# Kernel tuning notes

Hardware: AMD Instinct MI355X
Metric: run time of the kernel (lower is better)

## Reference

```python
import jax, jax.numpy as jnp
import numpy as np


def setup_inputs() -> dict:
    key = jax.random.key(0)
    k1, k2, k3 = jax.random.split(key, 3)
    B, D, F = 4096, 1024, 16384  # batch, input_dim, dict_size
    x = jax.random.normal(k1, (B, D), dtype=jnp.float32)
    W_enc = jax.random.normal(k2, (F, D), dtype=jnp.float32) * (1.0 / np.sqrt(D))
    b_enc = jnp.zeros((F,), dtype=jnp.float32)
    W_dec = jax.random.normal(k3, (D, F), dtype=jnp.float32)
    # decoder columns are unit-normalized (as in _normalize_decoder)
    W_dec = W_dec / jnp.clip(jnp.linalg.norm(W_dec, axis=0, keepdims=True), 1e-8)
    b_dec = jnp.zeros((D,), dtype=jnp.float32)
    return {"x": x, "W_enc": W_enc, "b_enc": b_enc, "W_dec": W_dec, "b_dec": b_dec, "k": 32}


def reference(x, W_enc, b_enc, W_dec, b_dec, k):
    # encode: z_pre = (x - b_dec) @ W_enc^T + b_enc   -> [B, F]
    x_centered = x - b_dec
    z_pre = jnp.einsum('bd,fd->bf', x_centered, W_enc) + b_enc
    # activate: TopK(ReLU(z_pre)) via top_k + relu + scatter
    topk_vals, topk_idx = jax.lax.top_k(z_pre, k)           # [B, k]
    B = z_pre.shape[0]
    rows = jnp.arange(B)[:, None]                            # [B, 1]
    z = jnp.zeros_like(z_pre).at[rows, topk_idx].set(jax.nn.relu(topk_vals))
    # decode: x_hat = z @ W_dec^T + b_dec (dense matmul over sparse z)
    x_hat = jnp.einsum('bf,df->bd', z, W_dec) + b_dec
    return (x_hat, z, z_pre)
```

## Files before the change

### kernel.cpp

```cpp
#include <hip/hip_runtime.h>
#include <cstdint>
#include <cfloat>
#include <cstddef>

#define MAXK 128

typedef __attribute__((ext_vector_type(8))) short bf16x8;
typedef __attribute__((ext_vector_type(4))) float f32x4;

__device__ __forceinline__ void split8(const float4& v0, const float4& v1,
                                       uint4& hp, uint4& lp)
{
    float vv[8] = {v0.x, v0.y, v0.z, v0.w, v1.x, v1.y, v1.z, v1.w};
    unsigned h[8], l[8];
    #pragma unroll
    for (int i = 0; i < 8; ++i) {
        unsigned u  = __float_as_uint(vv[i]);
        unsigned hb = u & 0xFFFF0000u;
        float lf    = vv[i] - __uint_as_float(hb);
        h[i] = u;
        l[i] = __float_as_uint(lf);
    }
    hp.x = (h[0] >> 16) | (h[1] & 0xFFFF0000u);
    hp.y = (h[2] >> 16) | (h[3] & 0xFFFF0000u);
    hp.z = (h[4] >> 16) | (h[5] & 0xFFFF0000u);
    hp.w = (h[6] >> 16) | (h[7] & 0xFFFF0000u);
    lp.x = (l[0] >> 16) | (l[1] & 0xFFFF0000u);
    lp.y = (l[2] >> 16) | (l[3] & 0xFFFF0000u);
    lp.z = (l[4] >> 16) | (l[5] & 0xFFFF0000u);
    lp.w = (l[6] >> 16) | (l[7] & 0xFFFF0000u);
}

__device__ __forceinline__ void gload_lds16(const void* g, void* l)
{
    __builtin_amdgcn_global_load_lds(
        (const __attribute__((address_space(1))) unsigned int*)g,
        (__attribute__((address_space(3))) unsigned int*)l,
        16, 0, 0);
}

__global__ __launch_bounds__(256)
void prep_x_kernel(const float* __restrict__ x, const float* __restrict__ b_dec,
                   ushort* __restrict__ AhiP, ushort* __restrict__ AloP, int D)
{
    const int c   = blockIdx.x * 256 + threadIdx.x;
    const int t   = c >> 9;
    const int wc  = c & 511;
    const int rl  = wc >> 2;
    const int pkc = wc & 3;
    const int kc  = (pkc - (rl >> 1)) & 3;
    const int nkb = D >> 5;
    const int band = t / nkb, kblk = t - band * nkb;
    const int row = band * 128 + rl;
    const int k0  = kblk * 32 + kc * 8;

    const float* src = x + (size_t)row * D + k0;
    float4 v0 = *(const float4*)(src);
    float4 v1 = *(const float4*)(src + 4);
    const float* bd = b_dec + k0;
    float4 d0 = *(const float4*)(bd);
    float4 d1 = *(const float4*)(bd + 4);
    v0.x -= d0.x; v0.y -= d0.y; v0.z -= d0.z; v0.w -= d0.w;
    v1.x -= d1.x; v1.y -= d1.y; v1.z -= d1.z; v1.w -= d1.w;
    uint4 hp, lp;
    split8(v0, v1, hp, lp);
    const size_t off = (size_t)t * 4096 + (size_t)wc * 8;
    *(uint4*)&AhiP[off] = hp;
    *(uint4*)&AloP[off] = lp;
}

__global__ __launch_bounds__(256)
void prep_w_kernel(const float* __restrict__ Wenc,
                   ushort* __restrict__ WhiP, ushort* __restrict__ WloP, int D)
{
    const int c   = blockIdx.x * 256 + threadIdx.x;
    const int t   = c >> 10;
    const int wc  = c & 1023;
    const int rl  = wc >> 2;
    const int pkc = wc & 3;
    const int kc  = (pkc - (rl >> 1)) & 3;
    const int nkb = D >> 5;
    const int fband = t / nkb, kblk = t - fband * nkb;
    const int f   = fband * 256 + rl;
    const int k0  = kblk * 32 + kc * 8;

    const float* src = Wenc + (size_t)f * D + k0;
    float4 v0 = *(const float4*)(src);
    float4 v1 = *(const float4*)(src + 4);
    uint4 hp, lp;
    split8(v0, v1, hp, lp);
    const size_t off = (size_t)t * 8192 + (size_t)wc * 8;
    *(uint4*)&WhiP[off] = hp;
    *(uint4*)&WloP[off] = lp;
}

__global__ __launch_bounds__(256, 2)
void encode_gemm_pre(const ushort* __restrict__ AhiP, const ushort* __restrict__ AloP,
                     const ushort* __restrict__ WhiP, const ushort* __restrict__ WloP,
                     const float* __restrict__ b_enc, float* __restrict__ z_pre,
                     int D, int F)
{
    __shared__ ushort AsHi[4096];
    __shared__ ushort AsLo[4096];
    __shared__ ushort BsHi[8192];
    __shared__ ushort BsLo[8192];

    const int tid = threadIdx.x;
    const int bm  = blockIdx.y * 128;
    const int bn  = blockIdx.x * 256;

    const int lane = tid & 63;
    const int w    = tid >> 6;
    const int wm   = (w >> 1) * 64;
    const int wn   = (w & 1) * 128;
    const int fr   = lane & 15;
    const int q    = lane >> 4;
    const int nkb  = D >> 5;

    int aoff[4], boff[8];
    #pragma unroll
    for (int mi = 0; mi < 4; ++mi) {
        const int r = wm + mi * 16 + fr;
        aoff[mi] = r * 32 + (((q + (r >> 1)) & 3) * 8);
    }
    #pragma unroll
    for (int ni = 0; ni < 8; ++ni) {
        const int r = wn + ni * 16 + fr;
        boff[ni] = r * 32 + (((q + (r >> 1)) & 3) * 8);
    }

    f32x4 acc[4][8];
    #pragma unroll
    for (int mi = 0; mi < 4; ++mi)
        #pragma unroll
        for (int ni = 0; ni < 8; ++ni)
            acc[mi][ni] = (f32x4){0.f, 0.f, 0.f, 0.f};

    const char* aHi = (const char*)AhiP + (size_t)blockIdx.y * nkb * 8192;
    const char* aLo = (const char*)AloP + (size_t)blockIdx.y * nkb * 8192;
    const char* bHi = (const char*)WhiP + (size_t)blockIdx.x * nkb * 16384;
    const char* bLo = (const char*)WloP + (size_t)blockIdx.x * nkb * 16384;
    const int la16 = lane * 16;

    for (int kb = 0; kb < nkb; ++kb) {
        const char* pa = aHi + (size_t)kb * 8192;
        const char* pl = aLo + (size_t)kb * 8192;
        const char* pb = bHi + (size_t)kb * 16384;
        const char* pm = bLo + (size_t)kb * 16384;

        #pragma unroll
        for (int c = 0; c < 2; ++c) {
            const int off = (w * 2 + c) * 1024;
            gload_lds16(pa + off + la16, (char*)AsHi + off);
            gload_lds16(pl + off + la16, (char*)AsLo + off);
        }
        #pragma unroll
        for (int c = 0; c < 4; ++c) {
            const int off = (w * 4 + c) * 1024;
            gload_lds16(pb + off + la16, (char*)BsHi + off);
            gload_lds16(pm + off + la16, (char*)BsLo + off);
        }
        asm volatile("s_waitcnt vmcnt(0)" ::: "memory");
        __syncthreads();

        bf16x8 ahi[4], alo[4];
        #pragma unroll
        for (int mi = 0; mi < 4; ++mi) {
            ahi[mi] = *(const bf16x8*)&AsHi[aoff[mi]];
            alo[mi] = *(const bf16x8*)&AsLo[aoff[mi]];
        }
        #pragma unroll
        for (int ni = 0; ni < 8; ++ni) {
            bf16x8 bhi = *(const bf16x8*)&BsHi[boff[ni]];
            bf16x8 blo = *(const bf16x8*)&BsLo[boff[ni]];
            #pragma unroll
            for (int mi = 0; mi < 4; ++mi) {
                acc[mi][ni] = __builtin_amdgcn_mfma_f32_16x16x32_bf16(alo[mi], bhi, acc[mi][ni], 0, 0, 0);
                acc[mi][ni] = __builtin_amdgcn_mfma_f32_16x16x32_bf16(ahi[mi], blo, acc[mi][ni], 0, 0, 0);
                acc[mi][ni] = __builtin_amdgcn_mfma_f32_16x16x32_bf16(ahi[mi], bhi, acc[mi][ni], 0, 0, 0);
            }
        }
        __syncthreads();
    }

    #pragma unroll
    for (int ni = 0; ni < 8; ++ni) {
        const int col = bn + wn + ni * 16 + fr;
        const float be = b_enc[col];
        #pragma unroll
        for (int mi = 0; mi < 4; ++mi) {
            const int rbase = bm + wm + mi * 16 + q * 4;
            float* dst = z_pre + (size_t)rbase * F + col;
            #pragma unroll
            for (int r = 0; r < 4; ++r)
                dst[(size_t)r * F] = acc[mi][ni][r] + be;
        }
    }
}

__global__ __launch_bounds__(256, 2)
void encode_gemm_bf16x3(const float* __restrict__ x, const float* __restrict__ Wenc,
                        const float* __restrict__ b_enc, const float* __restrict__ b_dec,
                        float* __restrict__ z_pre, int D, int F)
{
    constexpr int BM = 128, BN = 256, BK = 32;
    __shared__ ushort AsHi[BM * BK];
    __shared__ ushort AsLo[BM * BK];
    __shared__ ushort BsHi[BN * BK];
    __shared__ ushort BsLo[BN * BK];

    const int tid = threadIdx.x;
    const int bm  = blockIdx.y * BM;
    const int bn  = blockIdx.x * BN;

    const int lane = tid & 63;
    const int w    = tid >> 6;
    const int wm   = (w >> 1) * 64;
    const int wn   = (w & 1) * 128;
    const int fr   = lane & 15;
    const int q    = lane >> 4;

    int aoff[4], boff[8];
    #pragma unroll
    for (int mi = 0; mi < 4; ++mi) {
        const int r = wm + mi * 16 + fr;
        aoff[mi] = r * 32 + (((q + (r >> 1)) & 3) * 8);
    }
    #pragma unroll
    for (int ni = 0; ni < 8; ++ni) {
        const int r = wn + ni * 16 + fr;
        boff[ni] = r * 32 + (((q + (r >> 1)) & 3) * 8);
    }

    f32x4 acc[4][8];
    #pragma unroll
    for (int mi = 0; mi < 4; ++mi)
        #pragma unroll
        for (int ni = 0; ni < 8; ++ni)
            acc[mi][ni] = (f32x4){0.f, 0.f, 0.f, 0.f};

    for (int k0 = 0; k0 < D; k0 += BK) {
        #pragma unroll
        for (int j = 0; j < 2; ++j) {
            const int task = tid + 256 * j;
            const int row = task >> 2, kc = task & 3;
            const float* src = x + (size_t)(bm + row) * D + k0 + kc * 8;
            float4 v0 = *(const float4*)(src);
            float4 v1 = *(const float4*)(src + 4);
            const float* bd = b_dec + k0 + kc * 8;
            float4 d0 = *(const float4*)(bd);
            float4 d1 = *(const float4*)(bd + 4);
            v0.x -= d0.x; v0.y -= d0.y; v0.z -= d0.z; v0.w -= d0.w;
            v1.x -= d1.x; v1.y -= d1.y; v1.z -= d1.z; v1.w -= d1.w;
            uint4 hp, lp;
            split8(v0, v1, hp, lp);
            const int off = row * 32 + (((kc + (row >> 1)) & 3) * 8);
            *(uint4*)&AsHi[off] = hp;
            *(uint4*)&AsLo[off] = lp;
        }
        #pragma unroll
        for (int j = 0; j < 4; ++j) {
            const int task = tid + 256 * j;
            const int row = task >> 2, kc = task & 3;
            const float* src = Wenc + (size_t)(bn + row) * D + k0 + kc * 8;
            float4 v0 = *(const float4*)(src);
            float4 v1 = *(const float4*)(src + 4);
            uint4 hp, lp;
            split8(v0, v1, hp, lp);
            const int off = row * 32 + (((kc + (row >> 1)) & 3) * 8);
            *(uint4*)&BsHi[off] = hp;
            *(uint4*)&BsLo[off] = lp;
        }
        __syncthreads();

        bf16x8 ahi[4], alo[4];
        #pragma unroll
        for (int mi = 0; mi < 4; ++mi) {
            ahi[mi] = *(const bf16x8*)&AsHi[aoff[mi]];
            alo[mi] = *(const bf16x8*)&AsLo[aoff[mi]];
        }
        #pragma unroll
        for (int ni = 0; ni < 8; ++ni) {
            bf16x8 bhi = *(const bf16x8*)&BsHi[boff[ni]];
            bf16x8 blo = *(const bf16x8*)&BsLo[boff[ni]];
            #pragma unroll
            for (int mi = 0; mi < 4; ++mi) {
                acc[mi][ni] = __builtin_amdgcn_mfma_f32_16x16x32_bf16(alo[mi], bhi, acc[mi][ni], 0, 0, 0);
                acc[mi][ni] = __builtin_amdgcn_mfma_f32_16x16x32_bf16(ahi[mi], blo, acc[mi][ni], 0, 0, 0);
                acc[mi][ni] = __builtin_amdgcn_mfma_f32_16x16x32_bf16(ahi[mi], bhi, acc[mi][ni], 0, 0, 0);
            }
        }
        __syncthreads();
    }

    #pragma unroll
    for (int ni = 0; ni < 8; ++ni) {
        const int col = bn + wn + ni * 16 + fr;
        const float be = b_enc[col];
        #pragma unroll
        for (int mi = 0; mi < 4; ++mi) {
            const int rbase = bm + wm + mi * 16 + q * 4;
            float* dst = z_pre + (size_t)rbase * F + col;
            #pragma unroll
            for (int r = 0; r < 4; ++r)
                dst[(size_t)r * F] = acc[mi][ni][r] + be;
        }
    }
}

__device__ __forceinline__ unsigned fkey(float f)
{
    unsigned u = __float_as_uint(f);
    return u ^ ((unsigned)((int)u >> 31) | 0x80000000u);
}
__device__ __forceinline__ float finv(unsigned k)
{
    unsigned u = (k & 0x80000000u) ? (k ^ 0x80000000u) : ~k;
    return __uint_as_float(u);
}

__device__ __forceinline__ float exact_zpre(const float* __restrict__ xr,
                                            const float* __restrict__ Wenc,
                                            const float* __restrict__ b_enc,
                                            const float* __restrict__ b_dec,
                                            int f, int D, int ln)
{
    const float* wr = Wenc + (size_t)f * D;
    float s = 0.f;
    for (int d = ln * 4; d < D; d += 256) {
        float4 xv = *(const float4*)(xr + d);
        float4 bd = *(const float4*)(b_dec + d);
        float4 wv4 = *(const float4*)(wr + d);
        s = fmaf(xv.x - bd.x, wv4.x, s);
        s = fmaf(xv.y - bd.y, wv4.y, s);
        s = fmaf(xv.z - bd.z, wv4.z, s);
        s = fmaf(xv.w - bd.w, wv4.w, s);
    }
    #pragma unroll
    for (int o = 32; o > 0; o >>= 1) s += __shfl_down(s, o, 64);
    return s + b_enc[f];
}

#define DLT 4e-3f

template <int NVEC>
__global__ __launch_bounds__(256)
void topk_fast(const float* __restrict__ z_pre, float* __restrict__ z,
               float* __restrict__ ws_vals, int* __restrict__ ws_idx,
               const int* __restrict__ k_ptr,
               const float* __restrict__ x, const float* __restrict__ Wenc,
               const float* __restrict__ b_enc, const float* __restrict__ b_dec,
               int F, int D)
{
    const int row = blockIdx.x;
    const int t   = threadIdx.x;
    const int k   = *k_ptr;
    const int nv4 = F >> 2;
    const int wv_id = t >> 6, ln = t & 63;

    __shared__ ushort keys[16384];
    __shared__ float  cand_v[256];
    __shared__ int    cand_i[256];
    __shared__ unsigned char cand_sel[256];
    __shared__ int    bnd[128];
    __shared__ float  s2w[4];
    __shared__ int    hist4[4][256];
    __shared__ int    waveTot[4];
    __shared__ int    s_bin, s_above;
    __shared__ int    n_c_s, n_b_s, c_hi_s, out_cnt, cnt_tau_s, bad_s;
    __shared__ unsigned vk_key;

    if (t == 0) {
        n_c_s = 0; n_b_s = 0; c_hi_s = 0; out_cnt = 0; cnt_tau_s = 0; bad_s = 0;
        vk_key = 0xFFFFFFFFu;
    }

    const float*  zrow = z_pre + (size_t)row * F;
    const float4* src  = (const float4*)zrow;
    float4* dstz = (float4*)(z + (size_t)row * F);
    const float4 zz = make_float4(0.f, 0.f, 0.f, 0.f);

    float s2 = 0.f;
    #pragma unroll
    for (int i = 0; i < NVEC; ++i) {
        const int p = t + 256 * i;
        if (p < nv4) {
            const float4 v = src[p];
            dstz[p] = zz;
            const unsigned k0 = fkey(v.x) >> 16;
            const unsigned k1 = fkey(v.y) >> 16;
            const unsigned k2 = fkey(v.z) >> 16;
            const unsigned k3 = fkey(v.w) >> 16;
            uint2 pk;
            pk.x = k0 | (k1 << 16);
            pk.y = k2 | (k3 << 16);
            *(uint2*)&keys[p * 4] = pk;
            s2 = fmaf(v.x, v.x, s2);
            s2 = fmaf(v.y, v.y, s2);
            s2 = fmaf(v.z, v.z, s2);
            s2 = fmaf(v.w, v.w, s2);
        }
    }
    #pragma unroll
    for (int o = 32; o > 0; o >>= 1) s2 += __shfl_down(s2, o, 64);
    if (ln == 0) s2w[wv_id] = s2;
    __syncthreads();

    const float sigma = sqrtf((s2w[0] + s2w[1] + s2w[2] + s2w[3]) / (float)F);
    int c0 = 4 * k; if (c0 < 64) c0 = 64; if (c0 > 192) c0 = 192;
    const float qq  = (float)c0 / (float)F;
    const float tt  = sqrtf(-2.f * logf(qq));
    const float phi = tt - (2.30753f + 0.27061f * tt) /
                           (1.f + 0.99229f * tt + 0.04481f * tt * tt);
    const float tau = sigma * phi;
    const unsigned tk = fkey(tau) >> 16;
    const unsigned tkey16 = (tk >= 2) ? (tk - 2) : 0;

    const int nU = nv4 * 2;
    const unsigned* keysU = (const unsigned*)keys;
    for (int j = t; j < nU; j += 256) {
        const unsigned pr = keysU[j];
        const unsigned ka = pr & 0xFFFFu, kb = pr >> 16;
        if (ka > tkey16) { const int s = atomicAdd(&n_c_s, 1); if (s < 256) cand_i[s] = 2 * j; }
        if (kb > tkey16) { const int s = atomicAdd(&n_c_s, 1); if (s < 256) cand_i[s] = 2 * j + 1; }
    }
    __syncthreads();

    if (t == 0 && (n_c_s > 256 || !(tau > 0.1f))) bad_s = 1;
    const int n_c = min(n_c_s, 256);

    float myv = 0.f;
    if (t < n_c) {
        myv = zrow[cand_i[t]];
        cand_v[t] = myv;
        if (myv > tau) atomicAdd(&cnt_tau_s, 1);
    }
    __syncthreads();
    if (t == 0 && cnt_tau_s < k) bad_s = 1;

    cand_sel[t] = 0;
    if (t < n_c) {
        int gt = 0;
        for (int j = 0; j < n_c; ++j) gt += (cand_v[j] > myv);
        if (gt <= k - 1) atomicMin(&vk_key, fkey(myv));
    }
    __syncthreads();

    const float vkv = finv(vk_key);
    if (t < n_c) {
        if (myv > vkv + DLT) {
            cand_sel[t] = 2;
            atomicAdd(&c_hi_s, 1);
        } else if (myv > vkv - DLT) {
            const int sb = atomicAdd(&n_b_s, 1);
            if (sb < 128) bnd[sb] = t;
        }
    }
    __syncthreads();
    if (t == 0 && n_b_s > 128) bad_s = 1;
    __syncthreads();

    if (!bad_s) {
        const int n_b = n_b_s;
        const float* xr = x + (size_t)row * D;
        for (int b2 = wv_id; b2 < n_b; b2 += 4) {
            const int c = bnd[b2];
            const float ex = exact_zpre(xr, Wenc, b_enc, b_dec, cand_i[c], D, ln);
            if (ln == 0) cand_v[c] = ex;
        }
        __syncthreads();

        if (t == 0) {
            int need = k - c_hi_s;
            if (need > n_b) need = n_b;
            for (int it = 0; it < need; ++it) {
                int bi = -1; float bv = 0.f;
                for (int b2 = 0; b2 < n_b; ++b2) {
                    const int c = bnd[b2];
                    if (cand_sel[c]) continue;
                    const float v = cand_v[c];
                    if (bi < 0 || v > bv || (v == bv && cand_i[c] < cand_i[bi])) {
                        bi = c; bv = v;
                    }
                }
                if (bi < 0) break;
                cand_sel[bi] = 1;
            }
        }
        __syncthreads();

        float* wvp = ws_vals + (size_t)row * MAXK;
        int*   wip = ws_idx  + (size_t)row * MAXK;
        if (t < n_c && cand_sel[t]) {
            const float zv = fmaxf(cand_v[t], 0.f);
            z[(size_t)row * F + cand_i[t]] = zv;
            const int s = atomicAdd(&out_cnt, 1);
            if (s < MAXK) { wvp[s] = zv; wip[s] = cand_i[t]; }
        }
        return;
    }

    if (t == 0) { n_c_s = 0; c_hi_s = 0; out_cnt = 0; }
    __syncthreads();

    unsigned prefix = 0;
    int rem = k;
    for (int pass = 0; pass < 2; ++pass) {
        const int shift = 24 - 8 * pass;
        hist4[0][t] = 0; hist4[1][t] = 0; hist4[2][t] = 0; hist4[3][t] = 0;
        __syncthreads();
        for (int j = t; j < F; j += 256) {
            const unsigned key = fkey(zrow[j]);
            const bool inb = (pass == 0) || ((key >> (shift + 8)) == prefix);
            if (inb) atomicAdd(&hist4[wv_id][(key >> shift) & 255], 1);
        }
        __syncthreads();
        const int cnt = hist4[0][t] + hist4[1][t] + hist4[2][t] + hist4[3][t];
        int s = cnt;
        #pragma unroll
        for (int off = 1; off < 64; off <<= 1) {
            const int tmp = __shfl_down(s, off, 64);
            if (ln + off < 64) s += tmp;
        }
        if (ln == 0) waveTot[wv_id] = s;
        __syncthreads();
        int add = 0;
        #pragma unroll
        for (int w2 = 0; w2 < 4; ++w2)
            if (w2 > wv_id) add += waveTot[w2];
        const int sfx = s + add;
        const int nxt = sfx - cnt;
        if (sfx >= rem && nxt < rem) { s_bin = t; s_above = nxt; }
        __syncthreads();
        rem -= s_above;
        prefix = (prefix << 8) | (unsigned)s_bin;
        __syncthreads();
    }

    const float hiT = finv((prefix << 16) | 0xFFFFu) + DLT;
    const float loT = finv(prefix << 16) - DLT;

    for (int j = t; j < F; j += 256) {
        const float v = zrow[j];
        if (v > hiT) atomicAdd(&c_hi_s, 1);
        else if (v > loT) {
            const int s = atomicAdd(&n_c_s, 1);
            if (s < 256) { cand_i[s] = j; cand_sel[s] = 0; }
        }
    }
    __syncthreads();
    const int n_c2 = min(n_c_s, 256);

    {
        const float* xr = x + (size_t)row * D;
        for (int c = wv_id; c < n_c2; c += 4) {
            const float ex = exact_zpre(xr, Wenc, b_enc, b_dec, cand_i[c], D, ln);
            if (ln == 0) cand_v[c] = ex;
        }
    }
    __syncthreads();

    if (t == 0) {
        int need = k - c_hi_s;
        if (need > n_c2) need = n_c2;
        for (int it = 0; it < need; ++it) {
            int bi = -1; float bv = 0.f;
            for (int c = 0; c < n_c2; ++c) {
                if (cand_sel[c]) continue;
                const float v = cand_v[c];
                if (bi < 0 || v > bv || (v == bv && cand_i[c] < cand_i[bi])) {
                    bi = c; bv = v;
                }
            }
            if (bi < 0) break;
            cand_sel[bi] = 1;
        }
    }
    __syncthreads();

    {
        const float4 z4 = make_float4(0.f, 0.f, 0.f, 0.f);
        #pragma unroll
        for (int i = 0; i < NVEC; ++i) {
            const int p = t + 256 * i;
            if (p < nv4) dstz[p] = z4;
        }
    }
    __syncthreads();

    float* wvp = ws_vals + (size_t)row * MAXK;
    int*   wip = ws_idx  + (size_t)row * MAXK;
    for (int j = t; j < F; j += 256) {
        const float v = zrow[j];
        if (v > hiT) {
            const float zv = fmaxf(v, 0.f);
            z[(size_t)row * F + j] = zv;
            const int s = atomicAdd(&out_cnt, 1);
            if (s < MAXK) { wvp[s] = zv; wip[s] = j; }
        }
    }
    if (t < n_c2 && cand_sel[t]) {
        const float zv = fmaxf(cand_v[t], 0.f);
        z[(size_t)row * F + cand_i[t]] = zv;
        const int s = atomicAdd(&out_cnt, 1);
        if (s < MAXK) { wvp[s] = zv; wip[s] = cand_i[t]; }
    }
}

template <int NVEC>
__global__ __launch_bounds__(256)
void topk_kernel(const float* __restrict__ z_pre, float* __restrict__ z,
                 float* __restrict__ ws_vals, int* __restrict__ ws_idx,
                 const int* __restrict__ k_ptr,
                 const float* __restrict__ x, const float* __restrict__ Wenc,
                 const float* __restrict__ b_enc, const float* __restrict__ b_dec,
                 int F, int D)
{
    const int row = blockIdx.x;
    const int t   = threadIdx.x;
    const int k   = *k_ptr;
    const int nv4 = F >> 2;
    const int wv_id = t >> 6;
    const int ln    = t & 63;

    const float4* src = (const float4*)(z_pre + (size_t)row * F);
    float4 vals[NVEC];
    #pragma unroll
    for (int i = 0; i < NVEC; ++i) {
        const int p = t + 256 * i;
        if (p < nv4) vals[i] = src[p];
        else         vals[i] = make_float4(-FLT_MAX, -FLT_MAX, -FLT_MAX, -FLT_MAX);
    }

    __shared__ int hist[4][256];
    __shared__ int waveTot[4];
    __shared__ int s_bin, s_above;
    __shared__ int c_hi_s, n_c_s, out_cnt;
    __shared__ int cand_idx[128];
    __shared__ float cand_val[128];
    __shared__ unsigned char cand_sel[128];

    unsigned prefix = 0;
    int rem = k;

    #pragma unroll
    for (int pass = 0; pass < 2; ++pass) {
        const int shift = 24 - 8 * pass;
        hist[0][t] = 0; hist[1][t] = 0; hist[2][t] = 0; hist[3][t] = 0;
        __syncthreads();
        #pragma unroll
        for (int i = 0; i < NVEC; ++i) {
            const float* vv = (const float*)&vals[i];
            #pragma unroll
            for (int j = 0; j < 4; ++j) {
                const unsigned key = fkey(vv[j]);
                const bool inb = (pass == 0) || ((key >> (shift + 8)) == prefix);
                if (inb) atomicAdd(&hist[wv_id][(key >> shift) & 255], 1);
            }
        }
        __syncthreads();
        const int cnt = hist[0][t] + hist[1][t] + hist[2][t] + hist[3][t];
        int s = cnt;
        #pragma unroll
        for (int off = 1; off < 64; off <<= 1) {
            const int tmp = __shfl_down(s, off, 64);
            if (ln + off < 64) s += tmp;
        }
        if (ln == 0) waveTot[wv_id] = s;
        __syncthreads();
        int add = 0;
        #pragma unroll
        for (int w2 = 0; w2 < 4; ++w2)
            if (w2 > wv_id) add += waveTot[w2];
        const int sfx = s + add;
        const int nxt = sfx - cnt;
        if (sfx >= rem && nxt < rem) { s_bin = t; s_above = nxt; }
        __syncthreads();
        rem -= s_above;
        prefix = (prefix << 8) | (unsigned)s_bin;
        __syncthreads();
    }

    const unsigned keyLo = prefix << 16;
    const unsigned keyHi = keyLo | 0xFFFFu;
    const float dlt = 1e-3f;
    const float hiThr = finv(keyHi) + dlt;
    const float loThr = finv(keyLo) - dlt;

    if (t == 0) { c_hi_s = 0; n_c_s = 0; out_cnt = 0; }
    __syncthreads();

    #pragma unroll
    for (int i = 0; i < NVEC; ++i) {
        const float* vv = (const float*)&vals[i];
        #pragma unroll
        for (int j = 0; j < 4; ++j) {
            const float v = vv[j];
            if (v > hiThr) {
                atomicAdd(&c_hi_s, 1);
            } else if (v > loThr) {
                const int s = atomicAdd(&n_c_s, 1);
                if (s < 128) { cand_idx[s] = (t + 256 * i) * 4 + j; cand_sel[s] = 0; }
            }
        }
    }
    __syncthreads();

    const int n_c = min(n_c_s, 128);

    {
        const float* xr = x + (size_t)row * D;
        for (int c = wv_id; c < n_c; c += 4) {
            const float ex = exact_zpre(xr, Wenc, b_enc, b_dec, cand_idx[c], D, ln);
            if (ln == 0) cand_val[c] = ex;
        }
    }
    __syncthreads();

    if (t == 0) {
        int need = k - c_hi_s;
        if (need > n_c) need = n_c;
        for (int it = 0; it < need; ++it) {
            int bi = -1; float bv = 0.f;
            for (int c = 0; c < n_c; ++c) {
                if (cand_sel[c]) continue;
                const float v = cand_val[c];
                if (bi < 0 || v > bv || (v == bv && cand_idx[c] < cand_idx[bi])) {
                    bi = c; bv = v;
                }
            }
            if (bi < 0) break;
            cand_sel[bi] = 1;
        }
    }
    __syncthreads();

    float4* dstz = (float4*)(z + (size_t)row * F);
    float*  wv   = ws_vals + (size_t)row * MAXK;
    int*    wi   = ws_idx  + (size_t)row * MAXK;

    #pragma unroll
    for (int i = 0; i < NVEC; ++i) {
        const int p4 = t + 256 * i;
        if (p4 < nv4) {
            const float* vv = (const float*)&vals[i];
            float4 outv;
            float* ov = (float*)&outv;
            #pragma unroll
            for (int j = 0; j < 4; ++j) {
                const int pos = p4 * 4 + j;
                const float v = vv[j];
                float zv = 0.f;
                bool sel = false;
                if (v > hiThr) {
                    zv = fmaxf(v, 0.f); sel = true;
                } else if (v > loThr) {
                    for (int c = 0; c < n_c; ++c) {
                        if (cand_idx[c] == pos) {
                            if (cand_sel[c]) { zv = fmaxf(cand_val[c], 0.f); sel = true; }
                            break;
                        }
                    }
                }
                ov[j] = zv;
                if (sel) {
                    const int s = atomicAdd(&out_cnt, 1);
                    if (s < MAXK) { wv[s] = zv; wi[s] = pos; }
                }
            }
            dstz[p4] = outv;
        }
    }
}

__global__ __launch_bounds__(256)
void transpose4_kernel(const float* __restrict__ in, float* __restrict__ out,
                       int R, int C)
{
    __shared__ float tile[64][65];
    const int c0 = blockIdx.x * 64;
    const int r0 = blockIdx.y * 64;
    const int t  = threadIdx.x;
    const int tc = (t & 15) * 4;
    const int tr = t >> 4;

    #pragma unroll
    for (int i = 0; i < 4; ++i) {
        const int r = tr + i * 16;
        const float4 v = *(const float4*)(in + (size_t)(r0 + r) * C + c0 + tc);
        tile[r][tc]     = v.x;
        tile[r][tc + 1] = v.y;
        tile[r][tc + 2] = v.z;
        tile[r][tc + 3] = v.w;
    }
    __syncthreads();
    #pragma unroll
    for (int i = 0; i < 4; ++i) {
        const int c = tr + i * 16;
        float4 v;
        v.x = tile[tc]    [c];
        v.y = tile[tc + 1][c];
        v.z = tile[tc + 2][c];
        v.w = tile[tc + 3][c];
        *(float4*)(out + (size_t)(c0 + c) * R + r0 + tc) = v;
    }
}

__global__ __launch_bounds__(256)
void transpose_kernel(const float* __restrict__ in, float* __restrict__ out,
                      int R, int C)
{
    __shared__ float tile[32][33];
    const int c0 = blockIdx.x * 32;
    const int r0 = blockIdx.y * 32;
    const int tx = threadIdx.x & 31;
    const int ty = threadIdx.x >> 5;

    #pragma unroll
    for (int i = ty; i < 32; i += 8) {
        const int r = r0 + i, c = c0 + tx;
        tile[i][tx] = (r < R && c < C) ? in[(size_t)r * C + c] : 0.f;
    }
    __syncthreads();
    #pragma unroll
    for (int i = ty; i < 32; i += 8) {
        const int c = c0 + i, r = r0 + tx;
        if (c < C && r < R) out[(size_t)c * R + r] = tile[tx][i];
    }
}

__global__ __launch_bounds__(256)
void decode_kernel(const float* __restrict__ WdT, const float* __restrict__ wvals,
                   const int* __restrict__ widx, const float* __restrict__ b_dec,
                   float* __restrict__ x_hat, const int* __restrict__ k_ptr, int D)
{
    __shared__ float sv[MAXK];
    __shared__ int   si[MAXK];
    const int row = blockIdx.x;
    const int t   = threadIdx.x;
    int k = *k_ptr;
    if (k > MAXK) k = MAXK;

    if (t < MAXK) {
        sv[t] = wvals[(size_t)row * MAXK + t];
        si[t] = widx [(size_t)row * MAXK + t];
    }
    __syncthreads();

    for (int d0 = t * 4; d0 < D; d0 += 1024) {
        float4 a0 = *(const float4*)(b_dec + d0);
        float4 a1 = make_float4(0.f, 0.f, 0.f, 0.f);
        float4 a2 = make_float4(0.f, 0.f, 0.f, 0.f);
        float4 a3 = make_float4(0.f, 0.f, 0.f, 0.f);
        int j = 0;
        for (; j + 4 <= k; j += 4) {
            const float v0 = sv[j], v1 = sv[j+1], v2 = sv[j+2], v3 = sv[j+3];
            const float4 w0 = *(const float4*)(WdT + (size_t)si[j]   * D + d0);
            const float4 w1 = *(const float4*)(WdT + (size_t)si[j+1] * D + d0);
            const float4 w2 = *(const float4*)(WdT + (size_t)si[j+2] * D + d0);
            const float4 w3 = *(const float4*)(WdT + (size_t)si[j+3] * D + d0);
            a0.x = fmaf(v0, w0.x, a0.x); a0.y = fmaf(v0, w0.y, a0.y);
            a0.z = fmaf(v0, w0.z, a0.z); a0.w = fmaf(v0, w0.w, a0.w);
            a1.x = fmaf(v1, w1.x, a1.x); a1.y = fmaf(v1, w1.y, a1.y);
            a1.z = fmaf(v1, w1.z, a1.z); a1.w = fmaf(v1, w1.w, a1.w);
            a2.x = fmaf(v2, w2.x, a2.x); a2.y = fmaf(v2, w2.y, a2.y);
            a2.z = fmaf(v2, w2.z, a2.z); a2.w = fmaf(v2, w2.w, a2.w);
            a3.x = fmaf(v3, w3.x, a3.x); a3.y = fmaf(v3, w3.y, a3.y);
            a3.z = fmaf(v3, w3.z, a3.z); a3.w = fmaf(v3, w3.w, a3.w);
        }
        for (; j < k; ++j) {
            const float v0 = sv[j];
            const float4 w0 = *(const float4*)(WdT + (size_t)si[j] * D + d0);
            a0.x = fmaf(v0, w0.x, a0.x); a0.y = fmaf(v0, w0.y, a0.y);
            a0.z = fmaf(v0, w0.z, a0.z); a0.w = fmaf(v0, w0.w, a0.w);
        }
        a0.x += a1.x + a2.x + a3.x;
        a0.y += a1.y + a2.y + a3.y;
        a0.z += a1.z + a2.z + a3.z;
        a0.w += a1.w + a2.w + a3.w;
        *(float4*)(x_hat + (size_t)row * D + d0) = a0;
    }
}

extern "C" void kernel_launch(void* const* d_in, const int* in_sizes, int n_in,
                              void* d_out, int out_size, void* d_ws, size_t ws_size,
                              hipStream_t stream)
{
    const float* x     = (const float*)d_in[0];
    const float* W_enc = (const float*)d_in[1];
    const float* b_enc = (const float*)d_in[2];
    const float* W_dec = (const float*)d_in[3];
    const float* b_dec = (const float*)d_in[4];
    const int*   k_ptr = (const int*)d_in[5];

    const int F = in_sizes[2];
    const int D = in_sizes[4];
    const int B = in_sizes[0] / D;

    float* x_hat = (float*)d_out;
    float* z     = x_hat + (size_t)B * D;
    float* z_pre = z + (size_t)B * F;

    float* WdT = (float*)d_ws;
    float* wv  = WdT + (size_t)F * D;
    int*   wi  = (int*)(wv + (size_t)B * MAXK);
    char*  extra = (char*)(wi + (size_t)B * MAXK);

    const size_t base_need  = (size_t)F * D * 4 + (size_t)B * MAXK * 8;
    const size_t extra_need = (size_t)B * D * 4 + (size_t)F * D * 4;
    const bool use_pre = (ws_size >= base_need + extra_need) &&
                         (D % 32 == 0) && (B % 128 == 0) && (F % 256 == 0);

    if (use_pre) {
        ushort* AhiP = (ushort*)extra;
        ushort* AloP = AhiP + (size_t)B * D;
        ushort* WhiP = AloP + (size_t)B * D;
        ushort* WloP = WhiP + (size_t)F * D;

        prep_x_kernel<<<(B * (D / 8)) / 256, 256, 0, stream>>>(x, b_dec, AhiP, AloP, D);
        prep_w_kernel<<<(F * (D / 8)) / 256, 256, 0, stream>>>(W_enc, WhiP, WloP, D);
        encode_gemm_pre<<<dim3(F / 256, B / 128), 256, 0, stream>>>(
            AhiP, AloP, WhiP, WloP, b_enc, z_pre, D, F);
    } else {
        encode_gemm_bf16x3<<<dim3(F / 256, B / 128), 256, 0, stream>>>(
            x, W_enc, b_enc, b_dec, z_pre, D, F);
    }

    if ((D % 64 == 0) && (F % 64 == 0)) {
        transpose4_kernel<<<dim3(F / 64, D / 64), 256, 0, stream>>>(
            W_dec, WdT, D, F);
    } else {
        transpose_kernel<<<dim3((F + 31) / 32, (D + 31) / 32), 256, 0, stream>>>(
            W_dec, WdT, D, F);
    }

    const int nv4  = F / 4;
    const int nvec = (nv4 + 255) / 256;
    const bool fastok = (F <= 16384) && ((F & 3) == 0);

    if (fastok) {
        if (nvec <= 4)
            topk_fast<4><<<B, 256, 0, stream>>>(z_pre, z, wv, wi, k_ptr, x, W_enc, b_enc, b_dec, F, D);
        else if (nvec <= 8)
            topk_fast<8><<<B, 256, 0, stream>>>(z_pre, z, wv, wi, k_ptr, x, W_enc, b_enc, b_dec, F, D);
        else
            topk_fast<16><<<B, 256, 0, stream>>>(z_pre, z, wv, wi, k_ptr, x, W_enc, b_enc, b_dec, F, D);
    } else {
        if (nvec <= 8)
            topk_kernel<8><<<B, 256, 0, stream>>>(z_pre, z, wv, wi, k_ptr, x, W_enc, b_enc, b_dec, F, D);
        else if (nvec <= 16)
            topk_kernel<16><<<B, 256, 0, stream>>>(z_pre, z, wv, wi, k_ptr, x, W_enc, b_enc, b_dec, F, D);
        else
            topk_kernel<32><<<B, 256, 0, stream>>>(z_pre, z, wv, wi, k_ptr, x, W_enc, b_enc, b_dec, F, D);
    }

    decode_kernel<<<B, 256, 0, stream>>>(WdT, wv, wi, b_dec, x_hat, k_ptr, D);
}
```

Before: 1.106 ms.

## Estimate top-k threshold from input norm and drop LDS key staging

Replaces the top-k kernel with one that estimates the threshold tau from the centered x row norm instead of from a first pass over z_pre. This lets a single streaming pass over z_pre both zero the z output and collect candidates above a slightly lowered threshold, without the 32KB shared-memory key buffer. The aim is higher occupancy and less shared-memory traffic in the bandwidth-bound selection stage. The estimate relies on W_enc rows being roughly unit-scale random, so other weight distributions fall back to the slower radix-select path. The old topk_kernel variants and the templated dispatch are removed.

```diff
diff --git a/kernel.cpp b/kernel.cpp
--- a/kernel.cpp
+++ b/kernel.cpp
@@ -4,6 +4,8 @@
 #include <cstddef>
 
 #define MAXK 128
+#define FCAP 256
+#define DLT 4e-3f
 
 typedef __attribute__((ext_vector_type(8))) short bf16x8;
 typedef __attribute__((ext_vector_type(4))) float f32x4;
@@ -37,6 +39,39 @@
         (const __attribute__((address_space(1))) unsigned int*)g,
         (__attribute__((address_space(3))) unsigned int*)l,
         16, 0, 0);
+}
+
+__device__ __forceinline__ unsigned fkey(float f)
+{
+    unsigned u = __float_as_uint(f);
+    return u ^ ((unsigned)((int)u >> 31) | 0x80000000u);
+}
+__device__ __forceinline__ float finv(unsigned k)
+{
+    unsigned u = (k & 0x80000000u) ? (k ^ 0x80000000u) : ~k;
+    return __uint_as_float(u);
+}
+
+__device__ __forceinline__ float exact_zpre(const float* __restrict__ xr,
+                                            const float* __restrict__ Wenc,
+                                            const float* __restrict__ b_enc,
+                                            const float* __restrict__ b_dec,
+                                            int f, int D, int ln)
+{
+    const float* wr = Wenc + (size_t)f * D;
+    float s = 0.f;
+    for (int d = ln * 4; d < D; d += 256) {
+        float4 xv = *(const float4*)(xr + d);
+        float4 bd = *(const float4*)(b_dec + d);
+        float4 wv4 = *(const float4*)(wr + d);
+        s = fmaf(xv.x - bd.x, wv4.x, s);
+        s = fmaf(xv.y - bd.y, wv4.y, s);
+        s = fmaf(xv.z - bd.z, wv4.z, s);
+        s = fmaf(xv.w - bd.w, wv4.w, s);
+    }
+    #pragma unroll
+    for (int o = 32; o > 0; o >>= 1) s += __shfl_down(s, o, 64);
+    return s + b_enc[f];
 }
 
 __global__ __launch_bounds__(256)
@@ -308,97 +343,46 @@
     }
 }
 
-__device__ __forceinline__ unsigned fkey(float f)
-{
-    unsigned u = __float_as_uint(f);
-    return u ^ ((unsigned)((int)u >> 31) | 0x80000000u);
-}
-__device__ __forceinline__ float finv(unsigned k)
-{
-    unsigned u = (k & 0x80000000u) ? (k ^ 0x80000000u) : ~k;
-    return __uint_as_float(u);
-}
-
-__device__ __forceinline__ float exact_zpre(const float* __restrict__ xr,
-                                            const float* __restrict__ Wenc,
-                                            const float* __restrict__ b_enc,
-                                            const float* __restrict__ b_dec,
-                                            int f, int D, int ln)
-{
-    const float* wr = Wenc + (size_t)f * D;
-    float s = 0.f;
-    for (int d = ln * 4; d < D; d += 256) {
-        float4 xv = *(const float4*)(xr + d);
-        float4 bd = *(const float4*)(b_dec + d);
-        float4 wv4 = *(const float4*)(wr + d);
-        s = fmaf(xv.x - bd.x, wv4.x, s);
-        s = fmaf(xv.y - bd.y, wv4.y, s);
-        s = fmaf(xv.z - bd.z, wv4.z, s);
-        s = fmaf(xv.w - bd.w, wv4.w, s);
-    }
-    #pragma unroll
-    for (int o = 32; o > 0; o >>= 1) s += __shfl_down(s, o, 64);
-    return s + b_enc[f];
-}
-
-#define DLT 4e-3f
-
-template <int NVEC>
 __global__ __launch_bounds__(256)
-void topk_fast(const float* __restrict__ z_pre, float* __restrict__ z,
-               float* __restrict__ ws_vals, int* __restrict__ ws_idx,
-               const int* __restrict__ k_ptr,
-               const float* __restrict__ x, const float* __restrict__ Wenc,
-               const float* __restrict__ b_enc, const float* __restrict__ b_dec,
-               int F, int D)
+void topk_tau(const float* __restrict__ z_pre, float* __restrict__ z,
+              float* __restrict__ ws_vals, int* __restrict__ ws_idx,
+              const int* __restrict__ k_ptr,
+              const float* __restrict__ x, const float* __restrict__ Wenc,
+              const float* __restrict__ b_enc, const float* __restrict__ b_dec,
+              int F, int D)
 {
     const int row = blockIdx.x;
     const int t   = threadIdx.x;
     const int k   = *k_ptr;
-    const int nv4 = F >> 2;
     const int wv_id = t >> 6, ln = t & 63;
 
-    __shared__ ushort keys[16384];
-    __shared__ float  cand_v[256];
-    __shared__ int    cand_i[256];
-    __shared__ unsigned char cand_sel[256];
-    __shared__ int    bnd[128];
-    __shared__ float  s2w[4];
-    __shared__ int    hist4[4][256];
-    __shared__ int    waveTot[4];
-    __shared__ int    s_bin, s_above;
-    __shared__ int    n_c_s, n_b_s, c_hi_s, out_cnt, cnt_tau_s, bad_s;
+    __shared__ float s2w[4];
+    __shared__ float cand_v[FCAP];
+    __shared__ int   cand_i[FCAP];
+    __shared__ unsigned char cand_sel[FCAP];
+    __shared__ int   bnd[128];
+    __shared__ int   hist4[4][256];
+    __shared__ int   waveTot[4];
+    __shared__ int   s_bin, s_above;
+    __shared__ int   n_c_s, n_b_s, c_hi_s, out_cnt, cnt_tau_s, bad_s;
     __shared__ unsigned vk_key;
+    __shared__ float tau_sh, taulo_sh;
 
     if (t == 0) {
         n_c_s = 0; n_b_s = 0; c_hi_s = 0; out_cnt = 0; cnt_tau_s = 0; bad_s = 0;
         vk_key = 0xFFFFFFFFu;
     }
 
-    const float*  zrow = z_pre + (size_t)row * F;
-    const float4* src  = (const float4*)zrow;
-    float4* dstz = (float4*)(z + (size_t)row * F);
-    const float4 zz = make_float4(0.f, 0.f, 0.f, 0.f);
-
+    const float* xr = x + (size_t)row * D;
     float s2 = 0.f;
-    #pragma unroll
-    for (int i = 0; i < NVEC; ++i) {
-        const int p = t + 256 * i;
-        if (p < nv4) {
-            const float4 v = src[p];
-            dstz[p] = zz;
-            const unsigned k0 = fkey(v.x) >> 16;
-            const unsigned k1 = fkey(v.y) >> 16;
-            const unsigned k2 = fkey(v.z) >> 16;
-            const unsigned k3 = fkey(v.w) >> 16;
-            uint2 pk;
-            pk.x = k0 | (k1 << 16);
-            pk.y = k2 | (k3 << 16);
-            *(uint2*)&keys[p * 4] = pk;
-            s2 = fmaf(v.x, v.x, s2);
-            s2 = fmaf(v.y, v.y, s2);
-            s2 = fmaf(v.z, v.z, s2);
-            s2 = fmaf(v.w, v.w, s2);
+    if ((D & 3) == 0) {
+        for (int d = t * 4; d < D; d += 1024) {
+            float4 xv = *(const float4*)(xr + d);
+            float4 bd = *(const float4*)(b_dec + d);
+            const float a = xv.x - bd.x, b = xv.y - bd.y;
+            const float c = xv.z - bd.z, e = xv.w - bd.w;
+            s2 = fmaf(a, a, s2); s2 = fmaf(b, b, s2);
+            s2 = fmaf(c, c, s2); s2 = fmaf(e, e, s2);
         }
     }
     #pragma unroll
@@ -406,98 +390,124 @@
     if (ln == 0) s2w[wv_id] = s2;
     __syncthreads();
 
-    const float sigma = sqrtf((s2w[0] + s2w[1] + s2w[2] + s2w[3]) / (float)F);
-    int c0 = 4 * k; if (c0 < 64) c0 = 64; if (c0 > 192) c0 = 192;
-    const float qq  = (float)c0 / (float)F;
-    const float tt  = sqrtf(-2.f * logf(qq));
-    const float phi = tt - (2.30753f + 0.27061f * tt) /
-                           (1.f + 0.99229f * tt + 0.04481f * tt * tt);
-    const float tau = sigma * phi;
-    const unsigned tk = fkey(tau) >> 16;
-    const unsigned tkey16 = (tk >= 2) ? (tk - 2) : 0;
-
-    const int nU = nv4 * 2;
-    const unsigned* keysU = (const unsigned*)keys;
-    for (int j = t; j < nU; j += 256) {
-        const unsigned pr = keysU[j];
-        const unsigned ka = pr & 0xFFFFu, kb = pr >> 16;
-        if (ka > tkey16) { const int s = atomicAdd(&n_c_s, 1); if (s < 256) cand_i[s] = 2 * j; }
-        if (kb > tkey16) { const int s = atomicAdd(&n_c_s, 1); if (s < 256) cand_i[s] = 2 * j + 1; }
-    }
-    __syncthreads();
-
-    if (t == 0 && (n_c_s > 256 || !(tau > 0.1f))) bad_s = 1;
-    const int n_c = min(n_c_s, 256);
-
-    float myv = 0.f;
-    if (t < n_c) {
-        myv = zrow[cand_i[t]];
-        cand_v[t] = myv;
-        if (myv > tau) atomicAdd(&cnt_tau_s, 1);
-    }
-    __syncthreads();
-    if (t == 0 && cnt_tau_s < k) bad_s = 1;
-
+    if (t == 0) {
+        const float sig = sqrtf((s2w[0] + s2w[1] + s2w[2] + s2w[3]) / (float)D);
+        if (k <= 40 && F >= 4096 && sig > 1e-4f && (D & 3) == 0) {
+            const float qq  = 160.f / (float)F;
+            const float tt  = sqrtf(-2.f * logf(qq));
+            const float phi = tt - (2.30753f + 0.27061f * tt) /
+                                   (1.f + 0.99229f * tt + 0.04481f * tt * tt);
+            tau_sh   = sig * phi;
+            taulo_sh = tau_sh - 0.03f * sig;
+        } else {
+            tau_sh = -1.f; taulo_sh = FLT_MAX; bad_s = 1;
+        }
+    }
+    __syncthreads();
+    const float tau   = tau_sh;
+    const float taulo = taulo_sh;
+
+    const float* zrow = z_pre + (size_t)row * F;
+    float*       zout = z + (size_t)row * F;
+    const int nv4 = F >> 2;
+    {
+        const float4* src4 = (const float4*)zrow;
+        float4* dst4 = (float4*)zout;
+        const float4 zz = make_float4(0.f, 0.f, 0.f, 0.f);
+        for (int p = t; p < nv4; p += 256) {
+            const float4 v = src4[p];
+            dst4[p] = zz;
+            const float vv[4] = {v.x, v.y, v.z, v.w};
+            #pragma unroll
+            for (int j = 0; j < 4; ++j) {
+                if (vv[j] > taulo) {
+                    const int s = atomicAdd(&n_c_s, 1);
+                    if (s < FCAP) { cand_v[s] = vv[j]; cand_i[s] = p * 4 + j; }
+                    if (vv[j] > tau) atomicAdd(&cnt_tau_s, 1);
+                }
+            }
+        }
+        for (int p = nv4 * 4 + t; p < F; p += 256) {
+            const float v = zrow[p];
+            zout[p] = 0.f;
+            if (v > taulo) {
+                const int s = atomicAdd(&n_c_s, 1);
+                if (s < FCAP) { cand_v[s] = v; cand_i[s] = p; }
+                if (v > tau) atomicAdd(&cnt_tau_s, 1);
+            }
+        }
+    }
     cand_sel[t] = 0;
-    if (t < n_c) {
-        int gt = 0;
-        for (int j = 0; j < n_c; ++j) gt += (cand_v[j] > myv);
-        if (gt <= k - 1) atomicMin(&vk_key, fkey(myv));
-    }
-    __syncthreads();
-
-    const float vkv = finv(vk_key);
-    if (t < n_c) {
-        if (myv > vkv + DLT) {
-            cand_sel[t] = 2;
-            atomicAdd(&c_hi_s, 1);
-        } else if (myv > vkv - DLT) {
-            const int sb = atomicAdd(&n_b_s, 1);
-            if (sb < 128) bnd[sb] = t;
-        }
-    }
-    __syncthreads();
-    if (t == 0 && n_b_s > 128) bad_s = 1;
-    __syncthreads();
+    __syncthreads();
+
+    if (t == 0 && (n_c_s > FCAP || cnt_tau_s < k)) bad_s = 1;
+    __syncthreads();
+    const int n_c = min(n_c_s, FCAP);
+
+    float* wvp = ws_vals + (size_t)row * MAXK;
+    int*   wip = ws_idx  + (size_t)row * MAXK;
 
     if (!bad_s) {
-        const int n_b = n_b_s;
-        const float* xr = x + (size_t)row * D;
-        for (int b2 = wv_id; b2 < n_b; b2 += 4) {
-            const int c = bnd[b2];
-            const float ex = exact_zpre(xr, Wenc, b_enc, b_dec, cand_i[c], D, ln);
-            if (ln == 0) cand_v[c] = ex;
-        }
-        __syncthreads();
-
-        if (t == 0) {
-            int need = k - c_hi_s;
-            if (need > n_b) need = n_b;
-            for (int it = 0; it < need; ++it) {
-                int bi = -1; float bv = 0.f;
-                for (int b2 = 0; b2 < n_b; ++b2) {
-                    const int c = bnd[b2];
-                    if (cand_sel[c]) continue;
-                    const float v = cand_v[c];
-                    if (bi < 0 || v > bv || (v == bv && cand_i[c] < cand_i[bi])) {
-                        bi = c; bv = v;
+        float myv = -FLT_MAX;
+        if (t < n_c) myv = cand_v[t];
+
+        if (t < n_c) {
+            int gt = 0;
+            for (int j = 0; j < n_c; ++j) gt += (cand_v[j] > myv);
+            if (gt <= k - 1) atomicMin(&vk_key, fkey(myv));
+        }
+        __syncthreads();
+
+        const float vkv = finv(vk_key);
+        if (t < n_c) {
+            if (myv > vkv + DLT) {
+                cand_sel[t] = 2;
+                atomicAdd(&c_hi_s, 1);
+            } else if (myv > vkv - DLT) {
+                const int sb = atomicAdd(&n_b_s, 1);
+                if (sb < 128) bnd[sb] = t;
+            }
+        }
+        __syncthreads();
+        if (t == 0 && n_b_s > 128) bad_s = 1;
+        __syncthreads();
+
+        if (!bad_s) {
+            const int n_b = n_b_s;
+            for (int b2 = wv_id; b2 < n_b; b2 += 4) {
+                const int c = bnd[b2];
+                const float ex = exact_zpre(xr, Wenc, b_enc, b_dec, cand_i[c], D, ln);
+                if (ln == 0) cand_v[c] = ex;
+            }
+            __syncthreads();
+
+            if (t == 0) {
+                int need = k - c_hi_s;
+                if (need > n_b) need = n_b;
+                for (int it = 0; it < need; ++it) {
+                    int bi = -1; float bv = 0.f;
+                    for (int b2 = 0; b2 < n_b; ++b2) {
+                        const int c = bnd[b2];
+                        if (cand_sel[c]) continue;
+                        const float v = cand_v[c];
+                        if (bi < 0 || v > bv || (v == bv && cand_i[c] < cand_i[bi])) {
+                            bi = c; bv = v;
+                        }
                     }
+                    if (bi < 0) break;
+                    cand_sel[bi] = 1;
                 }
-                if (bi < 0) break;
-                cand_sel[bi] = 1;
-            }
-        }
-        __syncthreads();
-
-        float* wvp = ws_vals + (size_t)row * MAXK;
-        int*   wip = ws_idx  + (size_t)row * MAXK;
-        if (t < n_c && cand_sel[t]) {
-            const float zv = fmaxf(cand_v[t], 0.f);
-            z[(size_t)row * F + cand_i[t]] = zv;
-            const int s = atomicAdd(&out_cnt, 1);
-            if (s < MAXK) { wvp[s] = zv; wip[s] = cand_i[t]; }
-        }
-        return;
+            }
+            __syncthreads();
+
+            if (t < n_c && cand_sel[t]) {
+                const float zv = fmaxf(cand_v[t], 0.f);
+                zout[cand_i[t]] = zv;
+                const int s = atomicAdd(&out_cnt, 1);
+                if (s < MAXK) { wvp[s] = zv; wip[s] = cand_i[t]; }
+            }
+            return;
+        }
     }
 
     if (t == 0) { n_c_s = 0; c_hi_s = 0; out_cnt = 0; }
@@ -515,8 +525,8 @@
             if (inb) atomicAdd(&hist4[wv_id][(key >> shift) & 255], 1);
         }
         __syncthreads();
-        const int cnt = hist4[0][t] + hist4[1][t] + hist4[2][t] + hist4[3][t];
-        int s = cnt;
+        const int cnt2 = hist4[0][t] + hist4[1][t] + hist4[2][t] + hist4[3][t];
+        int s = cnt2;
         #pragma unroll
         for (int off = 1; off < 64; off <<= 1) {
             const int tmp = __shfl_down(s, off, 64);
@@ -529,7 +539,7 @@
         for (int w2 = 0; w2 < 4; ++w2)
             if (w2 > wv_id) add += waveTot[w2];
         const int sfx = s + add;
-        const int nxt = sfx - cnt;
+        const int nxt = sfx - cnt2;
         if (sfx >= rem && nxt < rem) { s_bin = t; s_above = nxt; }
         __syncthreads();
         rem -= s_above;
@@ -540,23 +550,22 @@
     const float hiT = finv((prefix << 16) | 0xFFFFu) + DLT;
     const float loT = finv(prefix << 16) - DLT;
 
+    cand_sel[t] = 0;
+    __syncthreads();
     for (int j = t; j < F; j += 256) {
         const float v = zrow[j];
         if (v > hiT) atomicAdd(&c_hi_s, 1);
         else if (v > loT) {
             const int s = atomicAdd(&n_c_s, 1);
-            if (s < 256) { cand_i[s] = j; cand_sel[s] = 0; }
-        }
-    }
-    __syncthreads();
-    const int n_c2 = min(n_c_s, 256);
-
-    {
-        const float* xr = x + (size_t)row * D;
-        for (int c = wv_id; c < n_c2; c += 4) {
-            const float ex = exact_zpre(xr, Wenc, b_enc, b_dec, cand_i[c], D, ln);
-            if (ln == 0) cand_v[c] = ex;
-        }
+            if (s < FCAP) { cand_i[s] = j; cand_sel[s] = 0; }
+        }
+    }
+    __syncthreads();
+    const int n_c2 = min(n_c_s, FCAP);
+
+    for (int c = wv_id; c < n_c2; c += 4) {
+        const float ex = exact_zpre(xr, Wenc, b_enc, b_dec, cand_i[c], D, ln);
+        if (ln == 0) cand_v[c] = ex;
     }
     __syncthreads();
 
@@ -578,198 +587,20 @@
     }
     __syncthreads();
 
-    {
-        const float4 z4 = make_float4(0.f, 0.f, 0.f, 0.f);
-        #pragma unroll
-        for (int i = 0; i < NVEC; ++i) {
-            const int p = t + 256 * i;
-            if (p < nv4) dstz[p] = z4;
-        }
-    }
-    __syncthreads();
-
-    float* wvp = ws_vals + (size_t)row * MAXK;
-    int*   wip = ws_idx  + (size_t)row * MAXK;
     for (int j = t; j < F; j += 256) {
         const float v = zrow[j];
         if (v > hiT) {
             const float zv = fmaxf(v, 0.f);
-            z[(size_t)row * F + j] = zv;
+            zout[j] = zv;
             const int s = atomicAdd(&out_cnt, 1);
             if (s < MAXK) { wvp[s] = zv; wip[s] = j; }
         }
     }
     if (t < n_c2 && cand_sel[t]) {
         const float zv = fmaxf(cand_v[t], 0.f);
-        z[(size_t)row * F + cand_i[t]] = zv;
+        zout[cand_i[t]] = zv;
         const int s = atomicAdd(&out_cnt, 1);
         if (s < MAXK) { wvp[s] = zv; wip[s] = cand_i[t]; }
-    }
-}
-
-template <int NVEC>
-__global__ __launch_bounds__(256)
-void topk_kernel(const float* __restrict__ z_pre, float* __restrict__ z,
-                 float* __restrict__ ws_vals, int* __restrict__ ws_idx,
-                 const int* __restrict__ k_ptr,
-                 const float* __restrict__ x, const float* __restrict__ Wenc,
-                 const float* __restrict__ b_enc, const float* __restrict__ b_dec,
-                 int F, int D)
-{
-    const int row = blockIdx.x;
-    const int t   = threadIdx.x;
-    const int k   = *k_ptr;
-    const int nv4 = F >> 2;
-    const int wv_id = t >> 6;
-    const int ln    = t & 63;
-
-    const float4* src = (const float4*)(z_pre + (size_t)row * F);
-    float4 vals[NVEC];
-    #pragma unroll
-    for (int i = 0; i < NVEC; ++i) {
-        const int p = t + 256 * i;
-        if (p < nv4) vals[i] = src[p];
-        else         vals[i] = make_float4(-FLT_MAX, -FLT_MAX, -FLT_MAX, -FLT_MAX);
-    }
-
-    __shared__ int hist[4][256];
-    __shared__ int waveTot[4];
-    __shared__ int s_bin, s_above;
-    __shared__ int c_hi_s, n_c_s, out_cnt;
-    __shared__ int cand_idx[128];
-    __shared__ float cand_val[128];
-    __shared__ unsigned char cand_sel[128];
-
-    unsigned prefix = 0;
-    int rem = k;
-
-    #pragma unroll
-    for (int pass = 0; pass < 2; ++pass) {
-        const int shift = 24 - 8 * pass;
-        hist[0][t] = 0; hist[1][t] = 0; hist[2][t] = 0; hist[3][t] = 0;
-        __syncthreads();
-        #pragma unroll
-        for (int i = 0; i < NVEC; ++i) {
-            const float* vv = (const float*)&vals[i];
-            #pragma unroll
-            for (int j = 0; j < 4; ++j) {
-                const unsigned key = fkey(vv[j]);
-                const bool inb = (pass == 0) || ((key >> (shift + 8)) == prefix);
-                if (inb) atomicAdd(&hist[wv_id][(key >> shift) & 255], 1);
-            }
-        }
-        __syncthreads();
-        const int cnt = hist[0][t] + hist[1][t] + hist[2][t] + hist[3][t];
-        int s = cnt;
-        #pragma unroll
-        for (int off = 1; off < 64; off <<= 1) {
-            const int tmp = __shfl_down(s, off, 64);
-            if (ln + off < 64) s += tmp;
-        }
-        if (ln == 0) waveTot[wv_id] = s;
-        __syncthreads();
-        int add = 0;
-        #pragma unroll
-        for (int w2 = 0; w2 < 4; ++w2)
-            if (w2 > wv_id) add += waveTot[w2];
-        const int sfx = s + add;
-        const int nxt = sfx - cnt;
-        if (sfx >= rem && nxt < rem) { s_bin = t; s_above = nxt; }
-        __syncthreads();
-        rem -= s_above;
-        prefix = (prefix << 8) | (unsigned)s_bin;
-        __syncthreads();
-    }
-
-    const unsigned keyLo = prefix << 16;
-    const unsigned keyHi = keyLo | 0xFFFFu;
-    const float dlt = 1e-3f;
-    const float hiThr = finv(keyHi) + dlt;
-    const float loThr = finv(keyLo) - dlt;
-
-    if (t == 0) { c_hi_s = 0; n_c_s = 0; out_cnt = 0; }
-    __syncthreads();
-
-    #pragma unroll
-    for (int i = 0; i < NVEC; ++i) {
-        const float* vv = (const float*)&vals[i];
-        #pragma unroll
-        for (int j = 0; j < 4; ++j) {
-            const float v = vv[j];
-            if (v > hiThr) {
-                atomicAdd(&c_hi_s, 1);
-            } else if (v > loThr) {
-                const int s = atomicAdd(&n_c_s, 1);
-                if (s < 128) { cand_idx[s] = (t + 256 * i) * 4 + j; cand_sel[s] = 0; }
-            }
-        }
-    }
-    __syncthreads();
-
-    const int n_c = min(n_c_s, 128);
-
-    {
-        const float* xr = x + (size_t)row * D;
-        for (int c = wv_id; c < n_c; c += 4) {
-            const float ex = exact_zpre(xr, Wenc, b_enc, b_dec, cand_idx[c], D, ln);
-            if (ln == 0) cand_val[c] = ex;
-        }
-    }
-    __syncthreads();
-
-    if (t == 0) {
-        int need = k - c_hi_s;
-        if (need > n_c) need = n_c;
-        for (int it = 0; it < need; ++it) {
-            int bi = -1; float bv = 0.f;
-            for (int c = 0; c < n_c; ++c) {
-                if (cand_sel[c]) continue;
-                const float v = cand_val[c];
-                if (bi < 0 || v > bv || (v == bv && cand_idx[c] < cand_idx[bi])) {
-                    bi = c; bv = v;
-                }
-            }
-            if (bi < 0) break;
-            cand_sel[bi] = 1;
-        }
-    }
-    __syncthreads();
-
-    float4* dstz = (float4*)(z + (size_t)row * F);
-    float*  wv   = ws_vals + (size_t)row * MAXK;
-    int*    wi   = ws_idx  + (size_t)row * MAXK;
-
-    #pragma unroll
-    for (int i = 0; i < NVEC; ++i) {
-        const int p4 = t + 256 * i;
-        if (p4 < nv4) {
-            const float* vv = (const float*)&vals[i];
-            float4 outv;
-            float* ov = (float*)&outv;
-            #pragma unroll
-            for (int j = 0; j < 4; ++j) {
-                const int pos = p4 * 4 + j;
-                const float v = vv[j];
-                float zv = 0.f;
-                bool sel = false;
-                if (v > hiThr) {
-                    zv = fmaxf(v, 0.f); sel = true;
-                } else if (v > loThr) {
-                    for (int c = 0; c < n_c; ++c) {
-                        if (cand_idx[c] == pos) {
-                            if (cand_sel[c]) { zv = fmaxf(cand_val[c], 0.f); sel = true; }
-                            break;
-                        }
-                    }
-                }
-                ov[j] = zv;
-                if (sel) {
-                    const int s = atomicAdd(&out_cnt, 1);
-                    if (s < MAXK) { wv[s] = zv; wi[s] = pos; }
-                }
-            }
-            dstz[p4] = outv;
-        }
     }
 }
 
@@ -926,33 +757,13 @@
             x, W_enc, b_enc, b_dec, z_pre, D, F);
     }
 
-    if ((D % 64 == 0) && (F % 64 == 0)) {
-        transpose4_kernel<<<dim3(F / 64, D / 64), 256, 0, stream>>>(
-            W_dec, WdT, D, F);
-    } else {
-        transpose_kernel<<<dim3((F + 31) / 32, (D + 31) / 32), 256, 0, stream>>>(
-            W_dec, WdT, D, F);
-    }
-
-    const int nv4  = F / 4;
-    const int nvec = (nv4 + 255) / 256;
-    const bool fastok = (F <= 16384) && ((F & 3) == 0);
-
-    if (fastok) {
-        if (nvec <= 4)
-            topk_fast<4><<<B, 256, 0, stream>>>(z_pre, z, wv, wi, k_ptr, x, W_enc, b_enc, b_dec, F, D);
-        else if (nvec <= 8)
-            topk_fast<8><<<B, 256, 0, stream>>>(z_pre, z, wv, wi, k_ptr, x, W_enc, b_enc, b_dec, F, D);
-        else
-            topk_fast<16><<<B, 256, 0, stream>>>(z_pre, z, wv, wi, k_ptr, x, W_enc, b_enc, b_dec, F, D);
-    } else {
-        if (nvec <= 8)
-            topk_kernel<8><<<B, 256, 0, stream>>>(z_pre, z, wv, wi, k_ptr, x, W_enc, b_enc, b_dec, F, D);
-        else if (nvec <= 16)
-            topk_kernel<16><<<B, 256, 0, stream>>>(z_pre, z, wv, wi, k_ptr, x, W_enc, b_enc, b_dec, F, D);
-        else
-            topk_kernel<32><<<B, 256, 0, stream>>>(z_pre, z, wv, wi, k_ptr, x, W_enc, b_enc, b_dec, F, D);
-    }
+    if ((D % 64 == 0) && (F % 64 == 0))
+        transpose4_kernel<<<dim3(F / 64, D / 64), 256, 0, stream>>>(W_dec, WdT, D, F);
+    else
+        transpose_kernel<<<dim3((F + 31) / 32, (D + 31) / 32), 256, 0, stream>>>(W_dec, WdT, D, F);
+
+    topk_tau<<<B, 256, 0, stream>>>(z_pre, z, wv, wi, k_ptr, x, W_enc,
+                                    b_enc, b_dec, F, D);
 
     decode_kernel<<<B, 256, 0, stream>>>(WdT, wv, wi, b_dec, x_hat, k_ptr, D);
 }
```

Result: no change. 1.091 ms (-1.4%).
